# Kernel tuning notes

Hardware: AMD Instinct MI355X
Metric: run time of the kernel (lower is better)

## Reference

```python
import jax, jax.numpy as jnp
import numpy as np

EPS = 1e-5
N_HEADS = 12

def _ln(x, w):
    x = x.astype(jnp.float32)
    m = jnp.mean(x, axis=-1, keepdims=True)
    v = jnp.mean((x - m) ** 2, axis=-1, keepdims=True)
    return (x - m) / jnp.sqrt(v + EPS) * w

def _rotate_half(x):
    x1, x2 = jnp.split(x, 2, axis=-1)
    return jnp.concatenate((-x2, x1), axis=-1)

def setup_inputs() -> dict:
    key = jax.random.key(0)
    ks = jax.random.split(key, 12)
    B, S, H, D, F = 2, 2048, 768, 64, 3072
    sc = 0.02
    return {
        'x': jax.random.normal(ks[0], (B, S, H), jnp.float32),
        'cos': jax.random.uniform(ks[1], (1, S, 1, 1, D), jnp.float32),
        'sin': jax.random.uniform(ks[2], (1, S, 1, 1, D), jnp.float32),
        'c': jax.random.normal(ks[3], (B, H), jnp.float32),
        'norm1_w': jnp.ones((H,), jnp.float32),
        'qkv_w': jax.random.normal(ks[4], (3 * H, H), jnp.float32) * sc,
        'attn_out_w': jax.random.normal(ks[5], (H, H), jnp.float32) * sc,
        'norm2_w': jnp.ones((H,), jnp.float32),
        'mlp_w1': jax.random.normal(ks[6], (F, H), jnp.float32) * sc,
        'mlp_b1': jax.random.normal(ks[7], (F,), jnp.float32) * sc,
        'mlp_w2': jax.random.normal(ks[8], (H, F), jnp.float32) * sc,
        'mlp_b2': jax.random.normal(ks[9], (H,), jnp.float32) * sc,
        'ada_w': jax.random.normal(ks[10], (6 * H, H), jnp.float32) * sc,
        'ada_b': jax.random.normal(ks[11], (6 * H,), jnp.float32) * sc,
    }

def reference(x, cos, sin, c, norm1_w, qkv_w, attn_out_w, norm2_w,
              mlp_w1, mlp_b1, mlp_w2, mlp_b2, ada_w, ada_b):
    B, S, H = x.shape
    h = N_HEADS
    d = H // h
    # adaLN modulation: [B, 6H] -> six [B, 1, H]
    mods = (c @ ada_w.T + ada_b)[:, None, :]
    shift_msa, scale_msa, gate_msa, shift_mlp, scale_mlp, gate_mlp = jnp.split(mods, 6, axis=2)
    x_skip = x
    xm = _ln(x, norm1_w) * (1 + scale_msa) + shift_msa
    qkv = (xm @ qkv_w.T).reshape(B, S, 3, h, d)
    q, k, v = qkv[:, :, 0], qkv[:, :, 1], qkv[:, :, 2]  # [B,S,h,d]
    # rotary: cos/sin [1,S,1,1,d] -> [1,S,1,d]
    cos2 = cos[0, :, 0, 0, :][None, :, None, :]
    sin2 = sin[0, :, 0, 0, :][None, :, None, :]
    q = q * cos2 + _rotate_half(q) * sin2
    k = k * cos2 + _rotate_half(k) * sin2
    scale = 1.0 / jnp.sqrt(jnp.float32(d))
    attn = jnp.einsum('bshd,bthd->bhst', q, k) * scale  # [B,h,S,S]
    attn = jax.nn.softmax(attn, axis=-1)
    # dropout: eval mode (training=False) -> identity
    o = jnp.einsum('bhst,bthd->bshd', attn, v).reshape(B, S, H)
    x1 = x_skip + gate_msa * (o @ attn_out_w.T)
    xm2 = _ln(x1, norm2_w) * (1 + scale_mlp) + shift_mlp
    hdn = jax.nn.gelu(xm2 @ mlp_w1.T + mlp_b1, approximate=True)
    y = hdn @ mlp_w2.T + mlp_b2
    return x1 + gate_mlp * y
```

## Files before the change

### kernel.cpp

```cpp
#include <hip/hip_runtime.h>

typedef __attribute__((ext_vector_type(8))) short short8;
typedef __attribute__((ext_vector_type(4))) float f32x4;
typedef __attribute__((ext_vector_type(16))) float f32x16;

#define S_LEN 2048
#define HID   768
#define NHEAD 12
#define HDIM  64
#define BATCH 2
#define MROWS (BATCH * S_LEN)
#define FFN   3072

static __device__ __forceinline__ float bf2f(unsigned short u) {
    unsigned int i = ((unsigned int)u) << 16;
    return __builtin_bit_cast(float, i);
}
static __device__ __forceinline__ unsigned short f2bf(float f) {
    unsigned int i = __builtin_bit_cast(unsigned int, f);
    unsigned int r = (i + 0x7FFFu + ((i >> 16) & 1u)) >> 16;
    return (unsigned short)r;
}

static __device__ __forceinline__ void gload16(const unsigned short* g, unsigned short* l) {
    __builtin_amdgcn_global_load_lds(
        (const __attribute__((address_space(1))) unsigned int*)(g),
        (__attribute__((address_space(3))) unsigned int*)(l), 16, 0, 0);
}

__global__ void wcvt_kernel(const float* __restrict__ qkv_w, const float* __restrict__ attn_w,
                            const float* __restrict__ mlp1, const float* __restrict__ mlp2,
                            unsigned short* __restrict__ o_qkv, unsigned short* __restrict__ o_attn,
                            unsigned short* __restrict__ o_mlp1, unsigned short* __restrict__ o_mlp2) {
    const int N0 = 3 * HID * HID / 4;
    const int N1 = N0 + HID * HID / 4;
    const int N2 = N1 + FFN * HID / 4;
    const int N3 = N2 + FFN * HID / 4;
    int i = blockIdx.x * 256 + threadIdx.x;
    const float* src; unsigned short* dst; int j;
    if (i < N0)      { src = qkv_w;  dst = o_qkv;  j = i; }
    else if (i < N1) { src = attn_w; dst = o_attn; j = i - N0; }
    else if (i < N2) { src = mlp1;   dst = o_mlp1; j = i - N1; }
    else if (i < N3) { src = mlp2;   dst = o_mlp2; j = i - N2; }
    else return;
    float4 v = ((const float4*)src)[j];
    ushort4 o;
    o.x = f2bf(v.x); o.y = f2bf(v.y); o.z = f2bf(v.z); o.w = f2bf(v.w);
    ((ushort4*)dst)[j] = o;
}

__global__ void ada_kernel(const float* __restrict__ c, const float* __restrict__ ada_w,
                           const float* __restrict__ ada_b, float* __restrict__ mods) {
    int j = blockIdx.x * 256 + threadIdx.x;
    if (j >= BATCH * 6 * HID) return;
    int b = j / (6 * HID), n = j % (6 * HID);
    const float* wr = ada_w + (size_t)n * HID;
    const float* cr = c + b * HID;
    float acc = 0.f;
    for (int k = 0; k < HID; k += 4) {
        float4 wv = *(const float4*)&wr[k];
        float4 cv = *(const float4*)&cr[k];
        acc += wv.x * cv.x + wv.y * cv.y + wv.z * cv.z + wv.w * cv.w;
    }
    mods[j] = acc + ada_b[n];
}

__global__ __launch_bounds__(256) void ln_mod_kernel(const float* __restrict__ in,
                                                     const float* __restrict__ w,
                                                     const float* __restrict__ mods,
                                                     int scale_off, int shift_off,
                                                     unsigned short* __restrict__ out) {
    int row = blockIdx.x;
    int b = row >> 11;
    int t = threadIdx.x;
    const float* xr = in + (size_t)row * HID;
    float v0 = xr[t], v1 = xr[t + 256], v2 = xr[t + 512];
    float s = v0 + v1 + v2;
    float s2 = v0 * v0 + v1 * v1 + v2 * v2;
    for (int m = 32; m > 0; m >>= 1) { s += __shfl_xor(s, m); s2 += __shfl_xor(s2, m); }
    __shared__ float reds[4], redq[4];
    int wid = t >> 6, lane = t & 63;
    if (lane == 0) { reds[wid] = s; redq[wid] = s2; }
    __syncthreads();
    float tot = reds[0] + reds[1] + reds[2] + reds[3];
    float tot2 = redq[0] + redq[1] + redq[2] + redq[3];
    float mean = tot * (1.0f / HID);
    float var = tot2 * (1.0f / HID) - mean * mean;
    float rstd = rsqrtf(var + 1e-5f);
    const float* mb = mods + b * (6 * HID);
    unsigned short* orow = out + (size_t)row * HID;
    float vv[3] = {v0, v1, v2};
    for (int i = 0; i < 3; i++) {
        int col = t + i * 256;
        float val = (vv[i] - mean) * rstd * w[col] * (1.0f + mb[scale_off + col]) + mb[shift_off + col];
        orow[col] = f2bf(val);
    }
}

__global__ __launch_bounds__(256) void ln2_fused_kernel(const float* __restrict__ x,
                                                        const unsigned short* __restrict__ p0,
                                                        const unsigned short* __restrict__ p1,
                                                        const float* __restrict__ w,
                                                        const float* __restrict__ mods,
                                                        float* __restrict__ x1out,
                                                        unsigned short* __restrict__ xm2) {
    int row = blockIdx.x;
    int b = row >> 11;
    int t = threadIdx.x;
    size_t ro = (size_t)row * HID;
    const float* mb = mods + b * (6 * HID);
    float v[3];
#pragma unroll
    for (int i = 0; i < 3; i++) {
        int col = t + i * 256;
        float pp = bf2f(p0[ro + col]) + bf2f(p1[ro + col]);
        v[i] = x[ro + col] + mb[1536 + col] * pp;
        x1out[ro + col] = v[i];
    }
    float s = v[0] + v[1] + v[2];
    float s2 = v[0] * v[0] + v[1] * v[1] + v[2] * v[2];
    for (int m = 32; m > 0; m >>= 1) { s += __shfl_xor(s, m); s2 += __shfl_xor(s2, m); }
    __shared__ float reds[4], redq[4];
    int wid = t >> 6, lane = t & 63;
    if (lane == 0) { reds[wid] = s; redq[wid] = s2; }
    __syncthreads();
    float tot = reds[0] + reds[1] + reds[2] + reds[3];
    float tot2 = redq[0] + redq[1] + redq[2] + redq[3];
    float mean = tot * (1.0f / HID);
    float var = tot2 * (1.0f / HID) - mean * mean;
    float rstd = rsqrtf(var + 1e-5f);
#pragma unroll
    for (int i = 0; i < 3; i++) {
        int col = t + i * 256;
        float val = (v[i] - mean) * rstd * w[col] * (1.0f + mb[3072 + col]) + mb[2304 + col];
        xm2[ro + col] = f2bf(val);
    }
}

template <int EPI, int NSPLIT>
__global__ __launch_bounds__(256) void gemm_bt(const unsigned short* __restrict__ A,
                                               const unsigned short* __restrict__ Bw,
                                               int M, int N, int K, int LDK,
                                               unsigned short* __restrict__ bout,
                                               unsigned short* __restrict__ pb1,
                                               unsigned short* __restrict__ pb2,
                                               unsigned short* __restrict__ pb3,
                                               const float* __restrict__ bias,
                                               unsigned short* __restrict__ vout,
                                               const float* __restrict__ cosb,
                                               const float* __restrict__ sinb) {
    __shared__ __align__(16) unsigned short a_lds[2 * 128 * 32];
    __shared__ __align__(16) unsigned short b_lds[2 * 128 * 32];
    int nxy = gridDim.x * gridDim.y;
    int bid = blockIdx.y * gridDim.x + blockIdx.x;
    int sw = (bid & 7) * (nxy >> 3) + (bid >> 3);
    int n0 = (sw % gridDim.x) * 128, m0 = (sw / gridDim.x) * 128;
    int z = (NSPLIT > 1) ? blockIdx.z : 0;
    unsigned short* ob = bout;
    if (NSPLIT > 1) {
        if (z == 1) ob = pb1; else if (z == 2) ob = pb2; else if (z == 3) ob = pb3;
    }
    int t = threadIdx.x, wid = t >> 6, lane = t & 63;
    int wr = wid >> 1, wc = wid & 1;
    int fr = lane & 15, kq = lane >> 4;
    f32x4 acc[4][4] = {};
    const unsigned short* ag = A + (size_t)(m0 + wid * 32 + (lane >> 2)) * LDK
                                 + (size_t)z * K + (lane & 3) * 8;
    const unsigned short* bg = Bw + (size_t)(n0 + wid * 32 + (lane >> 2)) * LDK
                                  + (size_t)z * K + (lane & 3) * 8;

    auto stage = [&](int buf, int k0) {
        unsigned short* al = a_lds + buf * 4096 + wid * 1024;
        unsigned short* bl = b_lds + buf * 4096 + wid * 1024;
        gload16(ag + k0, al);
        gload16(ag + k0 + (size_t)16 * LDK, al + 512);
        gload16(bg + k0, bl);
        gload16(bg + k0 + (size_t)16 * LDK, bl + 512);
    };

    int nt = K >> 5;
    stage(0, 0);
    asm volatile("s_waitcnt vmcnt(0)" ::: "memory");
    __builtin_amdgcn_s_barrier();
    for (int kt = 0; kt < nt; ++kt) {
        int cur = kt & 1;
        if (kt + 1 < nt) stage(cur ^ 1, (kt + 1) * 32);
        short8 af[4], bf4[4];
#pragma unroll
        for (int mm = 0; mm < 4; mm++)
            af[mm] = *(const short8*)&a_lds[cur * 4096 + (wr * 64 + mm * 16 + fr) * 32 + kq * 8];
#pragma unroll
        for (int nn = 0; nn < 4; nn++)
            bf4[nn] = *(const short8*)&b_lds[cur * 4096 + (wc * 64 + nn * 16 + fr) * 32 + kq * 8];
#pragma unroll
        for (int mm = 0; mm < 4; mm++)
#pragma unroll
            for (int nn = 0; nn < 4; nn++)
                acc[mm][nn] = __builtin_amdgcn_mfma_f32_16x16x32_bf16(af[mm], bf4[nn], acc[mm][nn], 0, 0, 0);
        asm volatile("s_waitcnt vmcnt(0)" ::: "memory");
        __builtin_amdgcn_s_barrier();
    }

    if (EPI == 4 && n0 < 2 * HID) {
        bool isq = (n0 < HID);
        const float SCQ = 0.125f * 1.44269504089f;
        unsigned short* dst = isq ? bout : pb1;
        int nb = n0 - (isq ? 0 : HID);
#pragma unroll
        for (int mm = 0; mm < 4; mm++) {
            int row0 = m0 + wr * 64 + mm * 16 + kq * 4;
            int bb = row0 >> 11, sA = row0 & (S_LEN - 1);
#pragma unroll
            for (int nn = 0; nn < 2; nn++) {
                int colq = nb + wc * 64 + nn * 16 + fr;
                int h = colq >> 6;
                int d = colq & 63;
                size_t hb = (size_t)(bb * NHEAD + h) * S_LEN;
#pragma unroll
                for (int r = 0; r < 4; r++) {
                    int s_ = sA + r;
                    float cs  = cosb[s_ * HDIM + d],      sn  = sinb[s_ * HDIM + d];
                    float cs2 = cosb[s_ * HDIM + d + 32], sn2 = sinb[s_ * HDIM + d + 32];
                    float a  = acc[mm][nn][r];
                    float a2 = acc[mm][nn + 2][r];
                    float o1 = a * cs - a2 * sn;
                    float o2 = a2 * cs2 + a * sn2;
                    if (isq) { o1 *= SCQ; o2 *= SCQ; }
                    size_t base = (hb + s_) * HDIM;
                    dst[base + d]      = f2bf(o1);
                    dst[base + d + 32] = f2bf(o2);
                }
            }
        }
    } else {
#pragma unroll
        for (int mm = 0; mm < 4; mm++)
#pragma unroll
            for (int nn = 0; nn < 4; nn++) {
                int row0 = m0 + wr * 64 + mm * 16 + kq * 4;
                int col = n0 + wc * 64 + nn * 16 + fr;
                if (EPI == 4) {
                    int vh = (col - 1536) >> 6, d = (col - 1536) & 63;
                    int bb = row0 >> 11, s0 = row0 & (S_LEN - 1);
                    ushort4 pk;
                    pk.x = f2bf(acc[mm][nn][0]);
                    pk.y = f2bf(acc[mm][nn][1]);
                    pk.z = f2bf(acc[mm][nn][2]);
                    pk.w = f2bf(acc[mm][nn][3]);
                    *(ushort4*)&vout[((size_t)(bb * NHEAD + vh) * HDIM + d) * S_LEN + s0] = pk;
                } else {
#pragma unroll
                    for (int r = 0; r < 4; r++) {
                        int row = row0 + r;
                        float v = acc[mm][nn][r];
                        size_t oi = (size_t)row * N + col;
                        if (EPI == 2) {
                            float hh = v + bias[col];
                            float u = 0.7978845608028654f * (hh + 0.044715f * hh * hh * hh);
                            float e = exp2f(2.885390082f * u);
                            float g = hh * (e * __builtin_amdgcn_rcpf(e + 1.0f));
                            ob[oi] = f2bf(g);
                        } else {
                            ob[oi] = f2bf(v);
                        }
                    }
                }
            }
    }
}

template <int NSPLIT, bool HASBIAS>
__global__ __launch_bounds__(256) void combine_kernel(const unsigned short* __restrict__ p0,
                                                      const unsigned short* __restrict__ p1,
                                                      const unsigned short* __restrict__ p2,
                                                      const unsigned short* __restrict__ p3,
                                                      const float* __restrict__ aux,
                                                      const float* __restrict__ mods,
                                                      int gate_off,
                                                      const float* __restrict__ bias,
                                                      float* __restrict__ out) {
    int i4 = blockIdx.x * 256 + threadIdx.x;
    if (i4 >= MROWS * HID / 4) return;
    int idx = i4 * 4;
    int row = idx / HID, col = idx - row * HID;
    int b = row >> 11;
    ushort4 u0 = *(const ushort4*)&p0[idx];
    ushort4 u1 = *(const ushort4*)&p1[idx];
    float s0 = bf2f(u0.x) + bf2f(u1.x);
    float s1 = bf2f(u0.y) + bf2f(u1.y);
    float s2 = bf2f(u0.z) + bf2f(u1.z);
    float s3 = bf2f(u0.w) + bf2f(u1.w);
    if (NSPLIT == 4) {
        ushort4 u2 = *(const ushort4*)&p2[idx];
        ushort4 u3 = *(const ushort4*)&p3[idx];
        s0 += bf2f(u2.x) + bf2f(u3.x);
        s1 += bf2f(u2.y) + bf2f(u3.y);
        s2 += bf2f(u2.z) + bf2f(u3.z);
        s3 += bf2f(u2.w) + bf2f(u3.w);
    }
    if (HASBIAS) {
        float4 bv = *(const float4*)&bias[col];
        s0 += bv.x; s1 += bv.y; s2 += bv.z; s3 += bv.w;
    }
    float4 ax = *(const float4*)&aux[idx];
    float4 gm = *(const float4*)&mods[b * (6 * HID) + gate_off + col];
    float4 o;
    o.x = ax.x + gm.x * s0;
    o.y = ax.y + gm.y * s1;
    o.z = ax.z + gm.z * s2;
    o.w = ax.w + gm.w * s3;
    *(float4*)&out[idx] = o;
}

__global__ __launch_bounds__(256) void attn_kernel(const unsigned short* __restrict__ qg,
                                                   const unsigned short* __restrict__ kg,
                                                   const unsigned short* __restrict__ vtg,
                                                   unsigned short* __restrict__ og) {
    int bh = blockIdx.y;
    int qt = blockIdx.x;
    int b = bh / NHEAD, h = bh % NHEAD;
    int t = threadIdx.x, wid = t >> 6, lane = t & 63;
    int l31 = lane & 31, hi = lane >> 5;
    int qsel = wid & 1, ksel = wid >> 1;

    union Smem {
        struct { unsigned short k[2][2][32 * 64]; unsigned short v[2][2][64 * 32]; } s;
        struct { float o[2][2][32][64]; float l[2][2][32]; } c;
    };
    __shared__ __align__(16) Smem sm;

    int qi = qt * 64 + qsel * 32 + l31;
    const unsigned short* qrow = qg + ((size_t)bh * S_LEN + qi) * HDIM;
    short8 qf[4];
#pragma unroll
    for (int ks = 0; ks < 4; ks++)
        qf[ks] = *(const short8*)&qrow[ks * 16 + hi * 8];

    f32x16 acc0 = {}, acc1 = {};
    float l_ = 0.f;

    const unsigned short* kbase = kg + (size_t)bh * S_LEN * HDIM;
    const unsigned short* vbase = vtg + (size_t)bh * HDIM * S_LEN;
    int kvb = ksel * (S_LEN / 2);

    auto stage = [&](int buf, int kv0) {
        if (qsel == 0) {
            unsigned short* kst = sm.s.k[ksel][buf];
#pragma unroll
            for (int g = 0; g < 4; g++)
                gload16(kbase + (size_t)(kv0 + g * 8 + (lane >> 3)) * HDIM
                              + (((lane & 7) ^ ((lane >> 3) & 7)) * 8),
                        kst + g * 512);
        } else {
            unsigned short* vst = sm.s.v[ksel][buf];
#pragma unroll
            for (int g = 0; g < 4; g++)
                gload16(vbase + (size_t)(g * 16 + (lane >> 2)) * S_LEN + kv0
                              + (((lane & 3) ^ ((lane >> 2) & 3)) * 8),
                        vst + g * 512);
        }
    };

    const int NT = (S_LEN / 2) / 32;
    stage(0, kvb);
    asm volatile("s_waitcnt vmcnt(0)" ::: "memory");
    __builtin_amdgcn_s_barrier();
    for (int kt = 0; kt < NT; kt++) {
        int cur = kt & 1;
        if (kt + 1 < NT) stage(cur ^ 1, kvb + (kt + 1) * 32);

        const unsigned short* kst = sm.s.k[ksel][cur];
        const unsigned short* vst = sm.s.v[ksel][cur];

        f32x16 s0 = {};
#pragma unroll
        for (int ks = 0; ks < 4; ks++) {
            short8 kf = *(const short8*)&kst[l31 * 64 + (((2 * ks + hi) ^ (l31 & 7)) * 8)];
            s0 = __builtin_amdgcn_mfma_f32_32x32x16_bf16(kf, qf[ks], s0, 0, 0, 0);
        }

#pragma unroll
        for (int i = 0; i < 16; i++) s0[i] = exp2f(s0[i]);

        float rs = ((s0[0] + s0[1]) + (s0[2] + s0[3])) + ((s0[4] + s0[5]) + (s0[6] + s0[7]))
                 + ((s0[8] + s0[9]) + (s0[10] + s0[11])) + ((s0[12] + s0[13]) + (s0[14] + s0[15]));
        l_ += rs;

#pragma unroll
        for (int c16 = 0; c16 < 2; c16++) {
            unsigned b0 = __builtin_bit_cast(unsigned, s0[c16 * 8 + 0]);
            unsigned b1 = __builtin_bit_cast(unsigned, s0[c16 * 8 + 1]);
            unsigned b2 = __builtin_bit_cast(unsigned, s0[c16 * 8 + 2]);
            unsigned b3 = __builtin_bit_cast(unsigned, s0[c16 * 8 + 3]);
            unsigned b4 = __builtin_bit_cast(unsigned, s0[c16 * 8 + 4]);
            unsigned b5 = __builtin_bit_cast(unsigned, s0[c16 * 8 + 5]);
            unsigned b6 = __builtin_bit_cast(unsigned, s0[c16 * 8 + 6]);
            unsigned b7 = __builtin_bit_cast(unsigned, s0[c16 * 8 + 7]);
            unsigned wv0 = (b1 & 0xFFFF0000u) | (b0 >> 16);
            unsigned wv1 = (b3 & 0xFFFF0000u) | (b2 >> 16);
            unsigned wv2 = (b5 & 0xFFFF0000u) | (b4 >> 16);
            unsigned wv3 = (b7 & 0xFFFF0000u) | (b6 >> 16);
            asm("v_permlane32_swap_b32 %0, %1" : "+v"(wv2), "+v"(wv0));
            asm("v_permlane32_swap_b32 %0, %1" : "+v"(wv3), "+v"(wv1));
            uint4 fw;
            fw.x = wv0; fw.y = wv1; fw.z = wv2; fw.w = wv3;
            short8 pa = __builtin_bit_cast(short8, fw);
            int ck = ((2 * c16 + hi) ^ (l31 & 3)) * 8;
            short8 vf0 = *(const short8*)&vst[l31 * 32 + ck];
            short8 vf1 = *(const short8*)&vst[(32 + l31) * 32 + ck];
            acc0 = __builtin_amdgcn_mfma_f32_32x32x16_bf16(pa, vf0, acc0, 0, 0, 0);
            acc1 = __builtin_amdgcn_mfma_f32_32x32x16_bf16(pa, vf1, acc1, 0, 0, 0);
        }

        asm volatile("s_waitcnt vmcnt(0)" ::: "memory");
        __builtin_amdgcn_s_barrier();
    }
    l_ += __shfl_xor(l_, 32);

#pragma unroll
    for (int r = 0; r < 16; r++) {
        int qr = (r & 3) + 8 * (r >> 2) + (hi << 2);
        sm.c.o[qsel][ksel][qr][l31] = acc0[r];
        sm.c.o[qsel][ksel][qr][32 + l31] = acc1[r];
    }
    if (hi == 0) sm.c.l[qsel][ksel][l31] = l_;
    __syncthreads();
#pragma unroll
    for (int i = 0; i < 16; i++) {
        int idx = i * 256 + t;
        int q = idx >> 6, d = idx & 63;
        int qs = q >> 5, qr = q & 31;
        float o = sm.c.o[qs][0][qr][d] + sm.c.o[qs][1][qr][d];
        float l = sm.c.l[qs][0][qr] + sm.c.l[qs][1][qr];
        og[((size_t)(b * S_LEN + qt * 64 + q)) * HID + h * HDIM + d] = f2bf(o / l);
    }
}

extern "C" void kernel_launch(void* const* d_in, const int* in_sizes, int n_in,
                              void* d_out, int out_size, void* d_ws, size_t ws_size,
                              hipStream_t stream) {
    const float* x          = (const float*)d_in[0];
    const float* cosb       = (const float*)d_in[1];
    const float* sinb       = (const float*)d_in[2];
    const float* c          = (const float*)d_in[3];
    const float* norm1_w    = (const float*)d_in[4];
    const float* qkv_w      = (const float*)d_in[5];
    const float* attn_out_w = (const float*)d_in[6];
    const float* norm2_w    = (const float*)d_in[7];
    const float* mlp_w1     = (const float*)d_in[8];
    const float* mlp_b1     = (const float*)d_in[9];
    const float* mlp_w2     = (const float*)d_in[10];
    const float* mlp_b2     = (const float*)d_in[11];
    const float* ada_w      = (const float*)d_in[12];
    const float* ada_b      = (const float*)d_in[13];
    float* out = (float*)d_out;

    char* p = (char*)d_ws;
    unsigned short* w_qkv  = (unsigned short*)p; p += (size_t)(3 * HID) * HID * 2;
    unsigned short* w_attn = (unsigned short*)p; p += (size_t)HID * HID * 2;
    unsigned short* w_mlp1 = (unsigned short*)p; p += (size_t)FFN * HID * 2;
    unsigned short* w_mlp2 = (unsigned short*)p; p += (size_t)HID * FFN * 2;
    float* mods            = (float*)p;          p += (size_t)BATCH * 6 * HID * 4;
    unsigned short* xm     = (unsigned short*)p; p += (size_t)MROWS * HID * 2;
    unsigned short* qkvb   = (unsigned short*)p; p += (size_t)MROWS * 3 * HID * 2;
    unsigned short* qb     = (unsigned short*)p; p += (size_t)MROWS * HID * 2;
    unsigned short* kb     = (unsigned short*)p; p += (size_t)MROWS * HID * 2;
    unsigned short* vtb    = (unsigned short*)p; p += (size_t)MROWS * HID * 2;
    unsigned short* ob  = xm;
    unsigned short* hdn = qkvb + (size_t)MROWS * HID;

    unsigned short* op0 = qkvb;
    unsigned short* op1 = qkvb + (size_t)MROWS * HID;
    unsigned short* xm2 = vtb;
    unsigned short* mp0 = xm;
    unsigned short* mp1 = qkvb;
    unsigned short* mp2 = vtb;
    unsigned short* mp3 = w_qkv;

    const int WCVT_N = (3 * HID * HID + HID * HID + 2 * FFN * HID) / 4;
    wcvt_kernel<<<(WCVT_N + 255) / 256, 256, 0, stream>>>(qkv_w, attn_out_w, mlp_w1, mlp_w2,
                                                          w_qkv, w_attn, w_mlp1, w_mlp2);
    ada_kernel<<<(BATCH * 6 * HID + 255) / 256, 256, 0, stream>>>(c, ada_w, ada_b, mods);
    ln_mod_kernel<<<MROWS, 256, 0, stream>>>(x, norm1_w, mods, HID, 0, xm);
    gemm_bt<4, 1><<<dim3(3 * HID / 128, MROWS / 128), 256, 0, stream>>>(
        xm, w_qkv, MROWS, 3 * HID, HID, HID, qb, kb, nullptr, nullptr, nullptr, vtb, cosb, sinb);
    attn_kernel<<<dim3(S_LEN / 64, BATCH * NHEAD), 256, 0, stream>>>(qb, kb, vtb, ob);
    gemm_bt<0, 2><<<dim3(HID / 128, MROWS / 128, 2), 256, 0, stream>>>(
        ob, w_attn, MROWS, HID, HID / 2, HID, op0, op1, nullptr, nullptr, nullptr, nullptr, nullptr, nullptr);
    ln2_fused_kernel<<<MROWS, 256, 0, stream>>>(x, op0, op1, norm2_w, mods, out, xm2);
    gemm_bt<2, 1><<<dim3(FFN / 128, MROWS / 128), 256, 0, stream>>>(
        xm2, w_mlp1, MROWS, FFN, HID, HID, hdn, nullptr, nullptr, nullptr, mlp_b1, nullptr, nullptr, nullptr);
    gemm_bt<0, 4><<<dim3(HID / 128, MROWS / 128, 4), 256, 0, stream>>>(
        hdn, w_mlp2, MROWS, HID, FFN / 4, FFN, mp0, mp1, mp2, mp3, nullptr, nullptr, nullptr, nullptr);
    combine_kernel<4, true><<<(MROWS * HID / 4 + 255) / 256, 256, 0, stream>>>(
        mp0, mp1, mp2, mp3, out, mods, 3840, mlp_b2, out);
}
```

Before: 220.7 us.

## Load attention K/V fragments directly from global memory and split KV across four waves

The attention kernel stops staging K and V tiles through double-buffered LDS with per-iteration barriers. Each wave now reads its MFMA operands straight from global memory (relying on L2/L1 for reuse) and processes a quarter of the key range for a 32-query tile. Block IDs are remapped so that blocks sharing a head are spread across XCDs. The grid doubles to 32-query tiles, and the final reduction combines four partial outputs. This removes LDS traffic and barrier stalls, but K/V is re-read from cache by every wave and block, with no software prefetch beyond what unrolling provides.

```diff
diff --git a/kernel.cpp b/kernel.cpp
--- a/kernel.cpp
+++ b/kernel.cpp
@@ -316,20 +316,19 @@
                                                    const unsigned short* __restrict__ kg,
                                                    const unsigned short* __restrict__ vtg,
                                                    unsigned short* __restrict__ og) {
-    int bh = blockIdx.y;
-    int qt = blockIdx.x;
+    int nb = gridDim.x * gridDim.y;
+    int bid = blockIdx.y * gridDim.x + blockIdx.x;
+    int nbid = (bid & 7) * (nb >> 3) + (bid >> 3);
+    int qt = nbid & 63;
+    int bh = nbid >> 6;
     int b = bh / NHEAD, h = bh % NHEAD;
     int t = threadIdx.x, wid = t >> 6, lane = t & 63;
     int l31 = lane & 31, hi = lane >> 5;
-    int qsel = wid & 1, ksel = wid >> 1;
-
-    union Smem {
-        struct { unsigned short k[2][2][32 * 64]; unsigned short v[2][2][64 * 32]; } s;
-        struct { float o[2][2][32][64]; float l[2][2][32]; } c;
-    };
-    __shared__ __align__(16) Smem sm;
-
-    int qi = qt * 64 + qsel * 32 + l31;
+
+    __shared__ __align__(16) float o_c[4][32][64];
+    __shared__ float l_c[4][32];
+
+    int qi = qt * 32 + l31;
     const unsigned short* qrow = qg + ((size_t)bh * S_LEN + qi) * HDIM;
     short8 qf[4];
 #pragma unroll
@@ -339,45 +338,30 @@
     f32x16 acc0 = {}, acc1 = {};
     float l_ = 0.f;
 
-    const unsigned short* kbase = kg + (size_t)bh * S_LEN * HDIM;
-    const unsigned short* vbase = vtg + (size_t)bh * HDIM * S_LEN;
-    int kvb = ksel * (S_LEN / 2);
-
-    auto stage = [&](int buf, int kv0) {
-        if (qsel == 0) {
-            unsigned short* kst = sm.s.k[ksel][buf];
-#pragma unroll
-            for (int g = 0; g < 4; g++)
-                gload16(kbase + (size_t)(kv0 + g * 8 + (lane >> 3)) * HDIM
-                              + (((lane & 7) ^ ((lane >> 3) & 7)) * 8),
-                        kst + g * 512);
-        } else {
-            unsigned short* vst = sm.s.v[ksel][buf];
-#pragma unroll
-            for (int g = 0; g < 4; g++)
-                gload16(vbase + (size_t)(g * 16 + (lane >> 2)) * S_LEN + kv0
-                              + (((lane & 3) ^ ((lane >> 2) & 3)) * 8),
-                        vst + g * 512);
-        }
-    };
-
-    const int NT = (S_LEN / 2) / 32;
-    stage(0, kvb);
-    asm volatile("s_waitcnt vmcnt(0)" ::: "memory");
-    __builtin_amdgcn_s_barrier();
-    for (int kt = 0; kt < NT; kt++) {
-        int cur = kt & 1;
-        if (kt + 1 < NT) stage(cur ^ 1, kvb + (kt + 1) * 32);
-
-        const unsigned short* kst = sm.s.k[ksel][cur];
-        const unsigned short* vst = sm.s.v[ksel][cur];
+    int kvb = wid * (S_LEN / 4);
+    const unsigned short* kp  = kg  + ((size_t)bh * S_LEN + kvb + l31) * HDIM + hi * 8;
+    const unsigned short* vp0 = vtg + ((size_t)bh * HDIM + l31) * S_LEN + kvb + hi * 8;
+    const unsigned short* vp1 = vtg + ((size_t)bh * HDIM + 32 + l31) * S_LEN + kvb + hi * 8;
+
+#pragma unroll 2
+    for (int kt = 0; kt < S_LEN / 4 / 32; kt++) {
+        short8 kf0 = *(const short8*)(kp);
+        short8 kf1 = *(const short8*)(kp + 16);
+        short8 kf2 = *(const short8*)(kp + 32);
+        short8 kf3 = *(const short8*)(kp + 48);
+        short8 va0 = *(const short8*)(vp0);
+        short8 va1 = *(const short8*)(vp0 + 16);
+        short8 vb0 = *(const short8*)(vp1);
+        short8 vb1 = *(const short8*)(vp1 + 16);
+        kp  += 32 * HDIM;
+        vp0 += 32;
+        vp1 += 32;
 
         f32x16 s0 = {};
-#pragma unroll
-        for (int ks = 0; ks < 4; ks++) {
-            short8 kf = *(const short8*)&kst[l31 * 64 + (((2 * ks + hi) ^ (l31 & 7)) * 8)];
-            s0 = __builtin_amdgcn_mfma_f32_32x32x16_bf16(kf, qf[ks], s0, 0, 0, 0);
-        }
+        s0 = __builtin_amdgcn_mfma_f32_32x32x16_bf16(kf0, qf[0], s0, 0, 0, 0);
+        s0 = __builtin_amdgcn_mfma_f32_32x32x16_bf16(kf1, qf[1], s0, 0, 0, 0);
+        s0 = __builtin_amdgcn_mfma_f32_32x32x16_bf16(kf2, qf[2], s0, 0, 0, 0);
+        s0 = __builtin_amdgcn_mfma_f32_32x32x16_bf16(kf3, qf[3], s0, 0, 0, 0);
 
 #pragma unroll
         for (int i = 0; i < 16; i++) s0[i] = exp2f(s0[i]);
@@ -405,34 +389,29 @@
             uint4 fw;
             fw.x = wv0; fw.y = wv1; fw.z = wv2; fw.w = wv3;
             short8 pa = __builtin_bit_cast(short8, fw);
-            int ck = ((2 * c16 + hi) ^ (l31 & 3)) * 8;
-            short8 vf0 = *(const short8*)&vst[l31 * 32 + ck];
-            short8 vf1 = *(const short8*)&vst[(32 + l31) * 32 + ck];
+            short8 vf0 = (c16 == 0) ? va0 : va1;
+            short8 vf1 = (c16 == 0) ? vb0 : vb1;
             acc0 = __builtin_amdgcn_mfma_f32_32x32x16_bf16(pa, vf0, acc0, 0, 0, 0);
             acc1 = __builtin_amdgcn_mfma_f32_32x32x16_bf16(pa, vf1, acc1, 0, 0, 0);
         }
-
-        asm volatile("s_waitcnt vmcnt(0)" ::: "memory");
-        __builtin_amdgcn_s_barrier();
     }
     l_ += __shfl_xor(l_, 32);
 
 #pragma unroll
     for (int r = 0; r < 16; r++) {
         int qr = (r & 3) + 8 * (r >> 2) + (hi << 2);
-        sm.c.o[qsel][ksel][qr][l31] = acc0[r];
-        sm.c.o[qsel][ksel][qr][32 + l31] = acc1[r];
-    }
-    if (hi == 0) sm.c.l[qsel][ksel][l31] = l_;
+        o_c[wid][qr][l31] = acc0[r];
+        o_c[wid][qr][32 + l31] = acc1[r];
+    }
+    if (hi == 0) l_c[wid][l31] = l_;
     __syncthreads();
 #pragma unroll
-    for (int i = 0; i < 16; i++) {
+    for (int i = 0; i < 8; i++) {
         int idx = i * 256 + t;
         int q = idx >> 6, d = idx & 63;
-        int qs = q >> 5, qr = q & 31;
-        float o = sm.c.o[qs][0][qr][d] + sm.c.o[qs][1][qr][d];
-        float l = sm.c.l[qs][0][qr] + sm.c.l[qs][1][qr];
-        og[((size_t)(b * S_LEN + qt * 64 + q)) * HID + h * HDIM + d] = f2bf(o / l);
+        float o = o_c[0][q][d] + o_c[1][q][d] + o_c[2][q][d] + o_c[3][q][d];
+        float l = l_c[0][q] + l_c[1][q] + l_c[2][q] + l_c[3][q];
+        og[((size_t)(b * S_LEN + qt * 32 + q)) * HID + h * HDIM + d] = f2bf(o / l);
     }
 }
 
@@ -484,7 +463,7 @@
     ln_mod_kernel<<<MROWS, 256, 0, stream>>>(x, norm1_w, mods, HID, 0, xm);
     gemm_bt<4, 1><<<dim3(3 * HID / 128, MROWS / 128), 256, 0, stream>>>(
         xm, w_qkv, MROWS, 3 * HID, HID, HID, qb, kb, nullptr, nullptr, nullptr, vtb, cosb, sinb);
-    attn_kernel<<<dim3(S_LEN / 64, BATCH * NHEAD), 256, 0, stream>>>(qb, kb, vtb, ob);
+    attn_kernel<<<dim3(S_LEN / 32, BATCH * NHEAD), 256, 0, stream>>>(qb, kb, vtb, ob);
     gemm_bt<0, 2><<<dim3(HID / 128, MROWS / 128, 2), 256, 0, stream>>>(
         ob, w_attn, MROWS, HID, HID / 2, HID, op0, op1, nullptr, nullptr, nullptr, nullptr, nullptr, nullptr);
     ln2_fused_kernel<<<MROWS, 256, 0, stream>>>(x, op0, op1, norm2_w, mods, out, xm2);
```

Result: slower. 258.5 us, median of 2 (+17.2%).
